# Optimization experiments

Measured on AMD Instinct MI355X. Metric: run time of the kernel, lower is better.

Reference implementation:

```python
import jax, jax.numpy as jnp
import numpy as np

# Module config (init_kwargs): nodes = (64, 64)
NX, NY_NODES = 64, 64


def setup_inputs() -> dict:
    key = jax.random.key(0)
    data = jax.random.normal(key, (4, 3, 1024, 1024), dtype=jnp.float32)
    return {"data": data}


def reference(data):
    B, C, H, W = data.shape
    scale = W // NX                    # = 16
    ny = H // scale                    # grid rows (= 64 here)
    nx = NX
    N = nx * ny                        # num_nodes = 4096
    p = scale - 1                      # original slices x1:x2 with x2=x1+scale-1 -> (scale-1) pixels

    # [B, C, ny, p, nx, p] top-left (scale-1)x(scale-1) sub-patch of each grid cell
    patches = data.reshape(B, C, ny, scale, nx, scale)[:, :, :, :p, :, :p]

    # L1 affinity between vertically / horizontally adjacent patches
    dv = jnp.abs(patches[:, :, 1:] - patches[:, :, :-1]).sum(axis=(1, 3, 5))          # [B, ny-1, nx]
    dh = jnp.abs(patches[:, :, :, :, 1:] - patches[:, :, :, :, :-1]).sum(axis=(1, 3, 5))  # [B, ny, nx-1]

    node = jnp.arange(ny)[:, None] * nx + jnp.arange(nx)[None, :]  # node_id = x + y*nx

    A = jnp.zeros((B, N, N), dtype=data.dtype)
    # vertical edges: self<->up/down
    lo_v = node[1:, :].ravel()   # lower cell of each vertical pair
    hi_v = node[:-1, :].ravel()  # upper cell
    dv_f = dv.reshape(B, -1)
    A = A.at[:, lo_v, hi_v].set(dv_f)   # self -> up
    A = A.at[:, hi_v, lo_v].set(dv_f)   # self -> down
    # horizontal edges: self<->left/right
    le_h = node[:, :-1].ravel()
    ri_h = node[:, 1:].ravel()
    dh_f = dh.reshape(B, -1)
    A = A.at[:, le_h, ri_h].set(dh_f)   # self -> right
    A = A.at[:, ri_h, le_h].set(dh_f)   # self -> left

    return A, data
```

## Files before the change

### kernel.cpp

```cpp
#include <hip/hip_runtime.h>

#define BB 4
#define CC 3
#define HH 1024
#define WW 1024
#define NXG 64
#define NYG 64
#define SCALE 16
#define PP 15
#define NNODE 4096

static const long long A_ELEMS    = (long long)BB * NNODE * NNODE;
static const long long DATA_ELEMS = (long long)BB * CC * HH * WW;

#define ROW_BLOCKS 4096
#define COPY_BLOCKS 1024

__global__ __launch_bounds__(256) void fused_kernel(const float* __restrict__ data,
                                                    float* __restrict__ out) {
    if (blockIdx.x < ROW_BLOCKS) {
        const int wid  = blockIdx.x * 4 + (threadIdx.x >> 6);
        const int lane = threadIdx.x & 63;
        const int b = wid >> 12;
        const int n = wid & (NNODE - 1);
        const int y = n >> 6;
        const int x = n & 63;

        const int r = lane >> 2;
        const int q = lane & 3;
        const bool active = (r < PP);

        const bool hasUp = y > 0, hasDown = y < NYG - 1;
        const bool hasLeft = x > 0, hasRight = x < NXG - 1;

        const float* cell = data + (((long long)(b * CC)) * HH + (long long)y * SCALE) * WW
                                 + x * SCALE;
        const long long CH = (long long)HH * WW;

        float sUp = 0.f, sDown = 0.f, sLeft = 0.f, sRight = 0.f;
        if (active) {
            #pragma unroll
            for (int c = 0; c < CC; ++c) {
                const float* p = cell + (long long)c * CH + (long long)r * WW + q * 4;
                const float4 cf = *(const float4*)p;
                const bool keepW = (q != 3);
                if (hasUp) {
                    float4 nf = *(const float4*)(p - (long long)SCALE * WW);
                    float d = fabsf(nf.x - cf.x) + fabsf(nf.y - cf.y) + fabsf(nf.z - cf.z);
                    if (keepW) d += fabsf(nf.w - cf.w);
                    sUp += d;
                }
                if (hasDown) {
                    float4 nf = *(const float4*)(p + (long long)SCALE * WW);
                    float d = fabsf(nf.x - cf.x) + fabsf(nf.y - cf.y) + fabsf(nf.z - cf.z);
                    if (keepW) d += fabsf(nf.w - cf.w);
                    sDown += d;
                }
                if (hasLeft) {
                    float4 nf = *(const float4*)(p - SCALE);
                    float d = fabsf(nf.x - cf.x) + fabsf(nf.y - cf.y) + fabsf(nf.z - cf.z);
                    if (keepW) d += fabsf(nf.w - cf.w);
                    sLeft += d;
                }
                if (hasRight) {
                    float4 nf = *(const float4*)(p + SCALE);
                    float d = fabsf(nf.x - cf.x) + fabsf(nf.y - cf.y) + fabsf(nf.z - cf.z);
                    if (keepW) d += fabsf(nf.w - cf.w);
                    sRight += d;
                }
            }
        }

        #pragma unroll
        for (int off = 1; off < 64; off <<= 1) {
            sUp    += __shfl_xor(sUp, off, 64);
            sDown  += __shfl_xor(sDown, off, 64);
            sLeft  += __shfl_xor(sLeft, off, 64);
            sRight += __shfl_xor(sRight, off, 64);
        }

        const int cUp    = hasUp    ? n - NXG : -1;
        const int cDown  = hasDown  ? n + NXG : -1;
        const int cLeft  = hasLeft  ? n - 1   : -1;
        const int cRight = hasRight ? n + 1   : -1;

        float4* rowp = (float4*)(out + (long long)b * NNODE * NNODE + (long long)n * NNODE);
        #pragma unroll
        for (int k = 0; k < 16; ++k) {
            const int f = k * 64 + lane;
            const int c0 = f * 4;
            float4 v;
            v.x = (c0   == cUp) ? sUp : (c0   == cLeft) ? sLeft : (c0   == cRight) ? sRight : (c0   == cDown) ? sDown : 0.f;
            v.y = (c0+1 == cUp) ? sUp : (c0+1 == cLeft) ? sLeft : (c0+1 == cRight) ? sRight : (c0+1 == cDown) ? sDown : 0.f;
            v.z = (c0+2 == cUp) ? sUp : (c0+2 == cLeft) ? sLeft : (c0+2 == cRight) ? sRight : (c0+2 == cDown) ? sDown : 0.f;
            v.w = (c0+3 == cUp) ? sUp : (c0+3 == cLeft) ? sLeft : (c0+3 == cRight) ? sRight : (c0+3 == cDown) ? sDown : 0.f;
            rowp[f] = v;
        }
    } else {
        long long i = (long long)(blockIdx.x - ROW_BLOCKS) * blockDim.x + threadIdx.x;
        const long long stride = (long long)COPY_BLOCKS * blockDim.x;
        const float4* __restrict__ src = (const float4*)data;
        float4* __restrict__ dst = (float4*)(out + A_ELEMS);
        const long long nvec = DATA_ELEMS / 4;
        for (; i < nvec; i += stride) dst[i] = src[i];
    }
}

extern "C" void kernel_launch(void* const* d_in, const int* in_sizes, int n_in,
                              void* d_out, int out_size, void* d_ws, size_t ws_size,
                              hipStream_t stream) {
    const float* data = (const float*)d_in[0];
    float* out = (float*)d_out;
    fused_kernel<<<ROW_BLOCKS + COPY_BLOCKS, 256, 0, stream>>>(data, out);
}
```

Baseline: 365.0 us.

## Split into edge-affinity kernel and row-writer kernel to avoid duplicate patch reads

Each edge affinity is now computed once by a dedicated wave and stored in a workspace buffer, where before each node recomputed all four neighbour sums. A second kernel writes each adjacency row, using wave-uniform indices to place the nonzero values. This removes the doubled data reads and the per-element compare chains in the row store. In exchange it adds a second launch and a dependency through the workspace. The run time is dominated by the 268MB output write, so the effect is likely small.

```diff
diff --git a/kernel.cpp b/kernel.cpp
--- a/kernel.cpp
+++ b/kernel.cpp
@@ -13,96 +13,113 @@
 static const long long A_ELEMS    = (long long)BB * NNODE * NNODE;
 static const long long DATA_ELEMS = (long long)BB * CC * HH * WW;
 
-#define ROW_BLOCKS 4096
-#define COPY_BLOCKS 1024
+#define NV_PER_B 4032
+#define NH_PER_B 4032
+#define NV_TOT   16128
+#define NE_TOT   32256
 
-__global__ __launch_bounds__(256) void fused_kernel(const float* __restrict__ data,
-                                                    float* __restrict__ out) {
-    if (blockIdx.x < ROW_BLOCKS) {
-        const int wid  = blockIdx.x * 4 + (threadIdx.x >> 6);
-        const int lane = threadIdx.x & 63;
-        const int b = wid >> 12;
-        const int n = wid & (NNODE - 1);
-        const int y = n >> 6;
-        const int x = n & 63;
+#define K1_COPY_BLOCKS 512
+#define K1_EDGE_BLOCKS 8064
 
-        const int r = lane >> 2;
-        const int q = lane & 3;
-        const bool active = (r < PP);
-
-        const bool hasUp = y > 0, hasDown = y < NYG - 1;
-        const bool hasLeft = x > 0, hasRight = x < NXG - 1;
-
-        const float* cell = data + (((long long)(b * CC)) * HH + (long long)y * SCALE) * WW
-                                 + x * SCALE;
-        const long long CH = (long long)HH * WW;
-
-        float sUp = 0.f, sDown = 0.f, sLeft = 0.f, sRight = 0.f;
-        if (active) {
-            #pragma unroll
-            for (int c = 0; c < CC; ++c) {
-                const float* p = cell + (long long)c * CH + (long long)r * WW + q * 4;
-                const float4 cf = *(const float4*)p;
-                const bool keepW = (q != 3);
-                if (hasUp) {
-                    float4 nf = *(const float4*)(p - (long long)SCALE * WW);
-                    float d = fabsf(nf.x - cf.x) + fabsf(nf.y - cf.y) + fabsf(nf.z - cf.z);
-                    if (keepW) d += fabsf(nf.w - cf.w);
-                    sUp += d;
-                }
-                if (hasDown) {
-                    float4 nf = *(const float4*)(p + (long long)SCALE * WW);
-                    float d = fabsf(nf.x - cf.x) + fabsf(nf.y - cf.y) + fabsf(nf.z - cf.z);
-                    if (keepW) d += fabsf(nf.w - cf.w);
-                    sDown += d;
-                }
-                if (hasLeft) {
-                    float4 nf = *(const float4*)(p - SCALE);
-                    float d = fabsf(nf.x - cf.x) + fabsf(nf.y - cf.y) + fabsf(nf.z - cf.z);
-                    if (keepW) d += fabsf(nf.w - cf.w);
-                    sLeft += d;
-                }
-                if (hasRight) {
-                    float4 nf = *(const float4*)(p + SCALE);
-                    float d = fabsf(nf.x - cf.x) + fabsf(nf.y - cf.y) + fabsf(nf.z - cf.z);
-                    if (keepW) d += fabsf(nf.w - cf.w);
-                    sRight += d;
-                }
-            }
-        }
-
-        #pragma unroll
-        for (int off = 1; off < 64; off <<= 1) {
-            sUp    += __shfl_xor(sUp, off, 64);
-            sDown  += __shfl_xor(sDown, off, 64);
-            sLeft  += __shfl_xor(sLeft, off, 64);
-            sRight += __shfl_xor(sRight, off, 64);
-        }
-
-        const int cUp    = hasUp    ? n - NXG : -1;
-        const int cDown  = hasDown  ? n + NXG : -1;
-        const int cLeft  = hasLeft  ? n - 1   : -1;
-        const int cRight = hasRight ? n + 1   : -1;
-
-        float4* rowp = (float4*)(out + (long long)b * NNODE * NNODE + (long long)n * NNODE);
-        #pragma unroll
-        for (int k = 0; k < 16; ++k) {
-            const int f = k * 64 + lane;
-            const int c0 = f * 4;
-            float4 v;
-            v.x = (c0   == cUp) ? sUp : (c0   == cLeft) ? sLeft : (c0   == cRight) ? sRight : (c0   == cDown) ? sDown : 0.f;
-            v.y = (c0+1 == cUp) ? sUp : (c0+1 == cLeft) ? sLeft : (c0+1 == cRight) ? sRight : (c0+1 == cDown) ? sDown : 0.f;
-            v.z = (c0+2 == cUp) ? sUp : (c0+2 == cLeft) ? sLeft : (c0+2 == cRight) ? sRight : (c0+2 == cDown) ? sDown : 0.f;
-            v.w = (c0+3 == cUp) ? sUp : (c0+3 == cLeft) ? sLeft : (c0+3 == cRight) ? sRight : (c0+3 == cDown) ? sDown : 0.f;
-            rowp[f] = v;
-        }
-    } else {
-        long long i = (long long)(blockIdx.x - ROW_BLOCKS) * blockDim.x + threadIdx.x;
-        const long long stride = (long long)COPY_BLOCKS * blockDim.x;
+__global__ __launch_bounds__(256) void edge_copy_kernel(const float* __restrict__ data,
+                                                        float* __restrict__ ws,
+                                                        float* __restrict__ out) {
+    if (blockIdx.x < K1_COPY_BLOCKS) {
+        long long i = (long long)blockIdx.x * 256 + threadIdx.x;
+        const long long stride = (long long)K1_COPY_BLOCKS * 256;
         const float4* __restrict__ src = (const float4*)data;
         float4* __restrict__ dst = (float4*)(out + A_ELEMS);
         const long long nvec = DATA_ELEMS / 4;
         for (; i < nvec; i += stride) dst[i] = src[i];
+        return;
+    }
+    const int wave = (blockIdx.x - K1_COPY_BLOCKS) * 4 + (threadIdx.x >> 6);
+    const int lane = threadIdx.x & 63;
+    const int r = lane >> 2;
+    const int q = lane & 3;
+
+    int b, y, x;
+    long long delta;
+    if (wave < NV_TOT) {
+        const int e = wave;
+        b = e / NV_PER_B; const int rem = e - b * NV_PER_B;
+        y = rem >> 6; x = rem & 63;
+        delta = (long long)SCALE * WW;
+    } else {
+        const int e = wave - NV_TOT;
+        b = e / NH_PER_B; const int rem = e - b * NH_PER_B;
+        y = rem / 63; x = rem - y * 63;
+        delta = SCALE;
+    }
+
+    const float* p0 = data + (((long long)(b * CC)) * HH + (long long)y * SCALE + r) * WW
+                           + x * SCALE + q * 4;
+    float s = 0.f;
+    if (r < PP) {
+        #pragma unroll
+        for (int c = 0; c < CC; ++c) {
+            const float* p = p0 + (long long)c * HH * WW;
+            const float4 a  = *(const float4*)p;
+            const float4 nb = *(const float4*)(p + delta);
+            float d = fabsf(nb.x - a.x) + fabsf(nb.y - a.y) + fabsf(nb.z - a.z);
+            if (q != 3) d += fabsf(nb.w - a.w);
+            s += d;
+        }
+    }
+    #pragma unroll
+    for (int off = 32; off; off >>= 1) s += __shfl_down(s, off, 64);
+    if (lane == 0) ws[wave] = s;
+}
+
+__global__ __launch_bounds__(256) void row_kernel(const float* __restrict__ ws,
+                                                  float* __restrict__ out) {
+    const int wid  = blockIdx.x * 4 + (threadIdx.x >> 6);
+    const int lane = threadIdx.x & 63;
+    const int b = wid >> 12;
+    const int n = wid & (NNODE - 1);
+    const int y = n >> 6, x = n & 63;
+
+    const bool hasUp = y > 0, hasDown = y < NYG - 1;
+    const bool hasLeft = x > 0, hasRight = x < NXG - 1;
+
+    float vUp = 0.f, vDown = 0.f, vLeft = 0.f, vRight = 0.f;
+    if (hasUp)    vUp    = ws[b * NV_PER_B + (y - 1) * 64 + x];
+    if (hasDown)  vDown  = ws[b * NV_PER_B + y * 64 + x];
+    if (hasLeft)  vLeft  = ws[NV_TOT + b * NH_PER_B + y * 63 + (x - 1)];
+    if (hasRight) vRight = ws[NV_TOT + b * NH_PER_B + y * 63 + x];
+
+    const int kUp    = __builtin_amdgcn_readfirstlane(hasUp    ? ((n - 64) >> 8) : -1);
+    const int kDown  = __builtin_amdgcn_readfirstlane(hasDown  ? ((n + 64) >> 8) : -1);
+    const int kLeft  = __builtin_amdgcn_readfirstlane(hasLeft  ? ((n - 1)  >> 8) : -1);
+    const int kRight = __builtin_amdgcn_readfirstlane(hasRight ? ((n + 1)  >> 8) : -1);
+    const int lUp    = __builtin_amdgcn_readfirstlane(((n - 64) >> 2) & 63);
+    const int lDown  = __builtin_amdgcn_readfirstlane(((n + 64) >> 2) & 63);
+    const int lLeft  = __builtin_amdgcn_readfirstlane(((n - 1)  >> 2) & 63);
+    const int lRight = __builtin_amdgcn_readfirstlane(((n + 1)  >> 2) & 63);
+
+    const int compUD = n & 3;
+    const int compL  = (n - 1) & 3;
+    const int compR  = (n + 1) & 3;
+
+    float4 pUp, pDown, pLeft, pRight;
+    pUp.x    = compUD == 0 ? vUp : 0.f;    pUp.y    = compUD == 1 ? vUp : 0.f;
+    pUp.z    = compUD == 2 ? vUp : 0.f;    pUp.w    = compUD == 3 ? vUp : 0.f;
+    pDown.x  = compUD == 0 ? vDown : 0.f;  pDown.y  = compUD == 1 ? vDown : 0.f;
+    pDown.z  = compUD == 2 ? vDown : 0.f;  pDown.w  = compUD == 3 ? vDown : 0.f;
+    pLeft.x  = compL == 0 ? vLeft : 0.f;   pLeft.y  = compL == 1 ? vLeft : 0.f;
+    pLeft.z  = compL == 2 ? vLeft : 0.f;   pLeft.w  = compL == 3 ? vLeft : 0.f;
+    pRight.x = compR == 0 ? vRight : 0.f;  pRight.y = compR == 1 ? vRight : 0.f;
+    pRight.z = compR == 2 ? vRight : 0.f;  pRight.w = compR == 3 ? vRight : 0.f;
+
+    float4* rowp = (float4*)(out + ((long long)b * NNODE + n) * NNODE);
+    #pragma unroll
+    for (int k = 0; k < 16; ++k) {
+        float4 v = make_float4(0.f, 0.f, 0.f, 0.f);
+        if (k == kUp)    { if (lane == lUp)    { v.x += pUp.x;    v.y += pUp.y;    v.z += pUp.z;    v.w += pUp.w;    } }
+        if (k == kDown)  { if (lane == lDown)  { v.x += pDown.x;  v.y += pDown.y;  v.z += pDown.z;  v.w += pDown.w;  } }
+        if (k == kLeft)  { if (lane == lLeft)  { v.x += pLeft.x;  v.y += pLeft.y;  v.z += pLeft.z;  v.w += pLeft.w;  } }
+        if (k == kRight) { if (lane == lRight) { v.x += pRight.x; v.y += pRight.y; v.z += pRight.z; v.w += pRight.w; } }
+        rowp[k * 64 + lane] = v;
     }
 }
 
@@ -111,5 +128,8 @@
                               hipStream_t stream) {
     const float* data = (const float*)d_in[0];
     float* out = (float*)d_out;
-    fused_kernel<<<ROW_BLOCKS + COPY_BLOCKS, 256, 0, stream>>>(data, out);
+    float* ws  = (float*)d_ws;
+
+    edge_copy_kernel<<<K1_COPY_BLOCKS + K1_EDGE_BLOCKS, 256, 0, stream>>>(data, ws, out);
+    row_kernel<<<4096, 256, 0, stream>>>(ws, out);
 }
```

Result: no change. 360.1 us (-1.4%).
